# Performance work log

Measured on AMD Instinct MI355X. Metric: run time of the kernel, lower is better.

The kernel has to match this reference:

```python
import jax, jax.numpy as jnp
import numpy as np

D_MODEL = 768
N_HEADS = 12
D_K = D_MODEL // N_HEADS
EPS = 1e-5


def layer_norm(x, g, b):
    mu = jnp.mean(x, axis=-1, keepdims=True)
    var = jnp.var(x, axis=-1, keepdims=True)
    return (x - mu) * jax.lax.rsqrt(var + EPS) * g + b


def setup_inputs() -> dict:
    key = jax.random.key(0)
    ks = jax.random.split(key, 16)
    d, h = D_MODEL, 4 * D_MODEL
    s = 1.0 / np.sqrt(d)
    inp = {
        "x": jax.random.normal(ks[0], (2, 4096, d), jnp.float32),
        "wq": jax.random.normal(ks[1], (d, d), jnp.float32) * s,
        "bq": jnp.zeros((d,), jnp.float32),
        "wk": jax.random.normal(ks[2], (d, d), jnp.float32) * s,
        "bk": jnp.zeros((d,), jnp.float32),
        "wv": jax.random.normal(ks[3], (d, d), jnp.float32) * s,
        "bv": jnp.zeros((d,), jnp.float32),
        "wo": jax.random.normal(ks[4], (d, d), jnp.float32) * s,
        "bo": jnp.zeros((d,), jnp.float32),
        "w1": jax.random.normal(ks[5], (h, d), jnp.float32) * s,
        "b1": jnp.zeros((h,), jnp.float32),
        "w2": jax.random.normal(ks[6], (d, h), jnp.float32) * (1.0 / np.sqrt(h)),
        "b2": jnp.zeros((d,), jnp.float32),
        "g1": jnp.ones((d,), jnp.float32),
        "beta1": jnp.zeros((d,), jnp.float32),
        "g2": jnp.ones((d,), jnp.float32),
        "beta2": jnp.zeros((d,), jnp.float32),
    }
    return inp


def reference(x, wq, bq, wk, bk, wv, bv, wo, bo, w1, b1, w2, b2, g1, beta1, g2, beta2):
    B, S, D = x.shape
    # --- MHA (self-attention, torch Linear: y = x @ W.T + b) ---
    def heads(t):  # [B,S,D] -> [B,H,S,d_k]
        return t.reshape(B, S, N_HEADS, D_K).transpose(0, 2, 1, 3)
    q = heads(x @ wq.T + bq)
    k = heads(x @ wk.T + bk)
    v = heads(x @ wv.T + bv)
    scores = jnp.einsum("bhqd,bhkd->bhqk", q, k) / np.sqrt(D_K)
    attn = jax.nn.softmax(scores, axis=-1)
    ctx = jnp.einsum("bhqk,bhkd->bhqd", attn, v)
    ctx = ctx.transpose(0, 2, 1, 3).reshape(B, S, D)
    mha_out = ctx @ wo.T + bo
    # --- residual + LN1 ---
    n1 = layer_norm(x + mha_out, g1, beta1)
    # --- FFN (exact GELU, dropout=0/eval) ---
    hdn = jax.nn.gelu(n1 @ w1.T + b1, approximate=False)
    ffn_out = hdn @ w2.T + b2
    # --- residual + LN2 ---
    return layer_norm(n1 + ffn_out, g2, beta2)
```

## Files before the change

kernel.cpp:

```cpp
#include <hip/hip_runtime.h>
#include <cstdint>
#include <cstddef>


#define D_MODEL 768
#define N_HEADS 12
#define D_K     64
#define SEQ     4096
#define BATCH   2
#define M_ROWS  (BATCH * SEQ)
#define H_FF    3072
#define LDQKV   2304

#define QSCALE 0.18033688011112042f

typedef __bf16 bf16_t;
typedef __attribute__((ext_vector_type(8))) __bf16 bf16x8;
typedef __attribute__((ext_vector_type(4))) __bf16 bf16x4;
typedef __attribute__((ext_vector_type(2))) __bf16 bf16x2;
typedef __attribute__((ext_vector_type(4))) float  floatx4;
typedef __attribute__((ext_vector_type(4))) short  short4_t;

union bf16x4_cast { bf16x4 h; short4_t s; };

__device__ __forceinline__ float gelu_exact(float x) {
    return 0.5f * x * (1.0f + erff(x * 0.70710678118654752f));
}

#if __has_builtin(__builtin_amdgcn_exp2f)
#define EXP2F(x) __builtin_amdgcn_exp2f(x)
#else
static __device__ __forceinline__ float EXP2F(float x) {
    float r; asm("v_exp_f32 %0, %1" : "=v"(r) : "v"(x)); return r;
}
#endif

#define GLL16(gp, lp)                                                         \
    __builtin_amdgcn_global_load_lds(                                         \
        (const __attribute__((address_space(1))) void*)(gp),                  \
        (__attribute__((address_space(3))) void*)(lp), 16, 0, 0)

#define NX_V  (6291456 / 4)
#define NW_V  (589824 / 4)
#define NF_V  (2359296 / 4)
#define NCONV_V (NX_V + 4 * NW_V + 2 * NF_V)

__global__ __launch_bounds__(256) void fused_convert_kernel(
    const float* __restrict__ x,  const float* __restrict__ wq,
    const float* __restrict__ wk, const float* __restrict__ wv,
    const float* __restrict__ wo, const float* __restrict__ w1,
    const float* __restrict__ w2,
    bf16_t* __restrict__ xb, bf16_t* __restrict__ wqkvb,
    bf16_t* __restrict__ wob, bf16_t* __restrict__ w1b,
    bf16_t* __restrict__ w2b) {
    const int v = blockIdx.x * 256 + threadIdx.x;
    const float* src; bf16_t* dst; int off; float scale = 1.0f;
    if (v < NX_V)                    { src = x;  dst = xb;              off = v; }
    else if (v < NX_V + NW_V)        { src = wq; dst = wqkvb;           off = v - NX_V; scale = QSCALE; }
    else if (v < NX_V + 2 * NW_V)    { src = wk; dst = wqkvb + 589824;  off = v - NX_V - NW_V; }
    else if (v < NX_V + 3 * NW_V)    { src = wv; dst = wqkvb + 1179648; off = v - NX_V - 2 * NW_V; }
    else if (v < NX_V + 4 * NW_V)    { src = wo; dst = wob;             off = v - NX_V - 3 * NW_V; }
    else if (v < NX_V + 4 * NW_V + NF_V) { src = w1; dst = w1b;         off = v - NX_V - 4 * NW_V; }
    else                             { src = w2; dst = w2b;             off = v - NX_V - 4 * NW_V - NF_V; }
    floatx4 f = *(const floatx4*)&src[(size_t)off * 4];
    bf16x4 o = bf16x4{(bf16_t)(f[0] * scale), (bf16_t)(f[1] * scale),
                      (bf16_t)(f[2] * scale), (bf16_t)(f[3] * scale)};
    *(bf16x4*)&dst[(size_t)off * 4] = o;
}

__global__ __launch_bounds__(256) void pack_bias_kernel(
    const float* __restrict__ bq, const float* __restrict__ bk,
    const float* __restrict__ bv, float* __restrict__ dst) {
    int i = blockIdx.x * 256 + threadIdx.x;
    if (i < 768)       dst[i] = bq[i] * QSCALE;
    else if (i < 1536) dst[i] = bk[i - 768];
    else if (i < 2304) dst[i] = bv[i - 1536];
}

template<int BN>
__global__ __launch_bounds__(256) void gemm_lds_kernel(
    const bf16_t* __restrict__ A, const bf16_t* __restrict__ W,
    const float* __restrict__ bias, bf16_t* __restrict__ C,
    int M, int N, int K, int act) {

    __shared__ bf16_t As[128 * 32];
    __shared__ bf16_t Bs[BN * 32];

    const int t    = threadIdx.x;
    const int lane = t & 63;
    const int w    = t >> 6;
    const int lrow = lane & 15;
    const int quad = lane >> 4;
    const int n0   = blockIdx.x * BN;
    const int m0   = blockIdx.y * 128;

    constexpr int MI  = (BN == 128) ? 4 : 2;
    const int wmo = (BN == 128) ? (w >> 1) * 64 : w * 32;
    const int wno = (BN == 128) ? (w & 1) * 64 : 0;

    const int aidx0 = (w * 2 + 0) * 64 + lane;
    const int aidx1 = (w * 2 + 1) * 64 + lane;
    const size_t a_g0 = (size_t)(m0 + (aidx0 >> 2)) * K + (aidx0 & 3) * 8;
    const size_t a_g1 = (size_t)(m0 + (aidx1 >> 2)) * K + (aidx1 & 3) * 8;
    size_t b_g0, b_g1 = 0;
    if constexpr (BN == 128) {
        b_g0 = (size_t)(n0 + (aidx0 >> 2)) * K + (aidx0 & 3) * 8;
        b_g1 = (size_t)(n0 + (aidx1 >> 2)) * K + (aidx1 & 3) * 8;
    } else {
        const int bidx = w * 64 + lane;
        b_g0 = (size_t)(n0 + (bidx >> 2)) * K + (bidx & 3) * 8;
    }

    floatx4 acc[MI][4];
#pragma unroll
    for (int i = 0; i < MI; ++i)
#pragma unroll
        for (int j = 0; j < 4; ++j) acc[i][j] = floatx4{0.f, 0.f, 0.f, 0.f};

    for (int k0 = 0; k0 < K; k0 += 32) {
        GLL16(&A[a_g0 + k0], &As[(w * 2 + 0) * 512]);
        GLL16(&A[a_g1 + k0], &As[(w * 2 + 1) * 512]);
        if constexpr (BN == 128) {
            GLL16(&W[b_g0 + k0], &Bs[(w * 2 + 0) * 512]);
            GLL16(&W[b_g1 + k0], &Bs[(w * 2 + 1) * 512]);
        } else {
            GLL16(&W[b_g0 + k0], &Bs[w * 512]);
        }
        __syncthreads();

        bf16x8 a[MI], b[4];
#pragma unroll
        for (int i = 0; i < MI; ++i)
            a[i] = *(bf16x8*)&As[(wmo + i * 16 + lrow) * 32 + quad * 8];
#pragma unroll
        for (int j = 0; j < 4; ++j)
            b[j] = *(bf16x8*)&Bs[(wno + j * 16 + lrow) * 32 + quad * 8];
#pragma unroll
        for (int i = 0; i < MI; ++i)
#pragma unroll
            for (int j = 0; j < 4; ++j)
                acc[i][j] = __builtin_amdgcn_mfma_f32_16x16x32_bf16(a[i], b[j], acc[i][j], 0, 0, 0);
        __syncthreads();
    }

#pragma unroll
    for (int i = 0; i < MI; ++i) {
#pragma unroll
        for (int j = 0; j < 4; ++j) {
            const int n = n0 + wno + j * 16 + lrow;
            const float bv = bias[n];
#pragma unroll
            for (int r = 0; r < 4; ++r) {
                const int m = m0 + wmo + i * 16 + quad * 4 + r;
                float v = acc[i][j][r] + bv;
                if (act) v = gelu_exact(v);
                C[(size_t)m * N + n] = (bf16_t)v;
            }
        }
    }
}

__global__ __launch_bounds__(256, 3) void attn_kernel(
    const bf16_t* __restrict__ QKV, bf16_t* __restrict__ Ctx) {

    __shared__ bf16_t Ks[64 * 72];
    __shared__ bf16_t Vt[64 * 72];

    const int t    = threadIdx.x;
    const int lane = t & 63;
    const int w    = t >> 6;
    const int lrow = lane & 15;
    const int quad = lane >> 4;

    const int b  = blockIdx.y / N_HEADS;
    const int h  = blockIdx.y % N_HEADS;
    const int q0 = blockIdx.x * 128 + w * 32;
    const size_t base_q = ((size_t)b * SEQ) * LDQKV + h * D_K;
    const size_t base_k = base_q + 768;
    const size_t base_v = base_q + 1536;
    const size_t base_o = ((size_t)b * SEQ) * D_MODEL + h * D_K;

    bf16x8 qf[2][2];
#pragma unroll
    for (int s = 0; s < 2; ++s) {
        const size_t qrow = base_q + (size_t)(q0 + s * 16 + lrow) * LDQKV + quad * 8;
        qf[s][0] = *(const bf16x8*)&QKV[qrow];
        qf[s][1] = *(const bf16x8*)&QKV[qrow + 32];
    }

    float l_part[2] = {0.f, 0.f};
    floatx4 o_acc[2][4];
#pragma unroll
    for (int s = 0; s < 2; ++s)
#pragma unroll
        for (int d = 0; d < 4; ++d) o_acc[s][d] = floatx4{0.f, 0.f, 0.f, 0.f};

    const int skey = t >> 2;
    const int sch  = t & 3;
    const int kp   = t >> 3;
    const int sch8 = t & 7;
    const int vcol = ((2 * kp) & 63) ^ (sch8 << 3);

    const size_t gk0 = base_k + (size_t)skey * LDQKV + sch * 8;
    const size_t gv0 = base_v + (size_t)(2 * kp) * LDQKV + sch8 * 8;
    bf16x8 kv0 = *(const bf16x8*)&QKV[gk0];
    bf16x8 kv1 = *(const bf16x8*)&QKV[gk0 + 32];
    bf16x8 vv0 = *(const bf16x8*)&QKV[gv0];
    bf16x8 vv1 = *(const bf16x8*)&QKV[gv0 + LDQKV];

    for (int k0 = 0; k0 < SEQ; k0 += 64) {
        *(bf16x8*)&Ks[skey * 72 + sch * 8]      = kv0;
        *(bf16x8*)&Ks[skey * 72 + sch * 8 + 32] = kv1;
#pragma unroll
        for (int j = 0; j < 8; ++j)
            *(bf16x2*)&Vt[(sch8 * 8 + j) * 72 + vcol] = bf16x2{vv0[j], vv1[j]};
        __syncthreads();

        if (k0 + 64 < SEQ) {
            const size_t gk = gk0 + (size_t)(k0 + 64) * LDQKV;
            const size_t gv = gv0 + (size_t)(k0 + 64) * LDQKV;
            kv0 = *(const bf16x8*)&QKV[gk];
            kv1 = *(const bf16x8*)&QKV[gk + 32];
            vv0 = *(const bf16x8*)&QKV[gv];
            vv1 = *(const bf16x8*)&QKV[gv + LDQKV];
        }

        __builtin_amdgcn_s_setprio(1);
        short4_t p[2][4];
#pragma unroll
        for (int kt = 0; kt < 4; ++kt) {
            bf16x8 ka0 = *(bf16x8*)&Ks[(kt * 16 + lrow) * 72 + quad * 8];
            bf16x8 ka1 = *(bf16x8*)&Ks[(kt * 16 + lrow) * 72 + 32 + quad * 8];
            floatx4 z = floatx4{0.f, 0.f, 0.f, 0.f};
#pragma unroll
            for (int s = 0; s < 2; ++s) {
                floatx4 st = __builtin_amdgcn_mfma_f32_16x16x32_bf16(ka0, qf[s][0], z, 0, 0, 0);
                st = __builtin_amdgcn_mfma_f32_16x16x32_bf16(ka1, qf[s][1], st, 0, 0, 0);
                float p0 = EXP2F(st[0]), p1 = EXP2F(st[1]);
                float p2 = EXP2F(st[2]), p3 = EXP2F(st[3]);
                l_part[s] += (p0 + p1) + (p2 + p3);
                bf16x4_cast pc;
                pc.h = bf16x4{(bf16_t)p0, (bf16_t)p1, (bf16_t)p2, (bf16_t)p3};
                p[s][kt] = pc.s;
            }
        }

#pragma unroll
        for (int dt = 0; dt < 4; ++dt) {
            const int d   = dt * 16 + lrow;
            const int swv = ((d >> 3) & 7) << 3;
#pragma unroll
            for (int kc = 0; kc < 4; ++kc) {
                bf16x4_cast ac;
                ac.h = *(bf16x4*)&Vt[d * 72 + ((kc * 16 + quad * 4) ^ swv)];
                o_acc[0][dt] = __builtin_amdgcn_mfma_f32_16x16x16bf16_1k(
                    ac.s, p[0][kc], o_acc[0][dt], 0, 0, 0);
                o_acc[1][dt] = __builtin_amdgcn_mfma_f32_16x16x16bf16_1k(
                    ac.s, p[1][kc], o_acc[1][dt], 0, 0, 0);
            }
        }
        __builtin_amdgcn_s_setprio(0);
        __syncthreads();
    }

#pragma unroll
    for (int s = 0; s < 2; ++s) {
        float lsum = l_part[s];
        lsum += __shfl_xor(lsum, 16, 64);
        lsum += __shfl_xor(lsum, 32, 64);
        const float inv = 1.0f / lsum;
        const size_t orow = base_o + (size_t)(q0 + s * 16 + lrow) * D_MODEL;
#pragma unroll
        for (int dt = 0; dt < 4; ++dt) {
            bf16x4 ov = bf16x4{(bf16_t)(o_acc[s][dt][0] * inv),
                               (bf16_t)(o_acc[s][dt][1] * inv),
                               (bf16_t)(o_acc[s][dt][2] * inv),
                               (bf16_t)(o_acc[s][dt][3] * inv)};
            *(bf16x4*)&Ctx[orow + dt * 16 + quad * 4] = ov;
        }
    }
}

__global__ __launch_bounds__(256) void ln_res_f32in_kernel(
    const float* __restrict__ x, const bf16_t* __restrict__ res,
    const float* __restrict__ g, const float* __restrict__ be,
    bf16_t* __restrict__ out) {
    const int row = blockIdx.x, t = threadIdx.x;
    const size_t base = (size_t)row * D_MODEL;
    float vals[3], sum = 0.f, sq = 0.f;
#pragma unroll
    for (int it = 0; it < 3; ++it) {
        int i = t + it * 256;
        float v = x[base + i] + (float)res[base + i];
        vals[it] = v; sum += v; sq += v * v;
    }
#pragma unroll
    for (int d = 1; d < 64; d <<= 1) { sum += __shfl_xor(sum, d, 64); sq += __shfl_xor(sq, d, 64); }
    __shared__ float ssum[4], ssq[4], s_mu, s_rs;
    if ((t & 63) == 0) { ssum[t >> 6] = sum; ssq[t >> 6] = sq; }
    __syncthreads();
    if (t == 0) {
        float S = ssum[0] + ssum[1] + ssum[2] + ssum[3];
        float Qq = ssq[0] + ssq[1] + ssq[2] + ssq[3];
        float mu = S / D_MODEL;
        s_mu = mu;
        s_rs = rsqrtf(Qq / D_MODEL - mu * mu + 1e-5f);
    }
    __syncthreads();
    const float mu = s_mu, rs = s_rs;
#pragma unroll
    for (int it = 0; it < 3; ++it) {
        int i = t + it * 256;
        out[base + i] = (bf16_t)((vals[it] - mu) * rs * g[i] + be[i]);
    }
}

__global__ __launch_bounds__(256) void ln_res_final_kernel(
    const bf16_t* __restrict__ a, const bf16_t* __restrict__ bfb,
    const float* __restrict__ g, const float* __restrict__ be,
    float* __restrict__ out) {
    const int row = blockIdx.x, t = threadIdx.x;
    const size_t base = (size_t)row * D_MODEL;
    float vals[3], sum = 0.f, sq = 0.f;
#pragma unroll
    for (int it = 0; it < 3; ++it) {
        int i = t + it * 256;
        float v = (float)a[base + i] + (float)bfb[base + i];
        vals[it] = v; sum += v; sq += v * v;
    }
#pragma unroll
    for (int d = 1; d < 64; d <<= 1) { sum += __shfl_xor(sum, d, 64); sq += __shfl_xor(sq, d, 64); }
    __shared__ float ssum[4], ssq[4], s_mu, s_rs;
    if ((t & 63) == 0) { ssum[t >> 6] = sum; ssq[t >> 6] = sq; }
    __syncthreads();
    if (t == 0) {
        float S = ssum[0] + ssum[1] + ssum[2] + ssum[3];
        float Qq = ssq[0] + ssq[1] + ssq[2] + ssq[3];
        float mu = S / D_MODEL;
        s_mu = mu;
        s_rs = rsqrtf(Qq / D_MODEL - mu * mu + 1e-5f);
    }
    __syncthreads();
    const float mu = s_mu, rs = s_rs;
#pragma unroll
    for (int it = 0; it < 3; ++it) {
        int i = t + it * 256;
        out[base + i] = (vals[it] - mu) * rs * g[i] + be[i];
    }
}

extern "C" void kernel_launch(void* const* d_in, const int* in_sizes, int n_in,
                              void* d_out, int out_size, void* d_ws, size_t ws_size,
                              hipStream_t stream) {
    const float* x    = (const float*)d_in[0];
    const float* wq   = (const float*)d_in[1];
    const float* bq   = (const float*)d_in[2];
    const float* wk   = (const float*)d_in[3];
    const float* bk   = (const float*)d_in[4];
    const float* wv   = (const float*)d_in[5];
    const float* bv   = (const float*)d_in[6];
    const float* wo   = (const float*)d_in[7];
    const float* bo   = (const float*)d_in[8];
    const float* w1   = (const float*)d_in[9];
    const float* b1   = (const float*)d_in[10];
    const float* w2   = (const float*)d_in[11];
    const float* b2   = (const float*)d_in[12];
    const float* g1   = (const float*)d_in[13];
    const float* be1  = (const float*)d_in[14];
    const float* g2   = (const float*)d_in[15];
    const float* be2  = (const float*)d_in[16];
    float* out = (float*)d_out;

    char* ws = (char*)d_ws;
    const size_t SZ_XB   = (size_t)M_ROWS * D_MODEL * 2;
    const size_t SZ_QKV  = (size_t)M_ROWS * LDQKV * 2;
    const size_t SZ_CTX  = SZ_XB;
    const size_t SZ_H    = (size_t)M_ROWS * H_FF * 2;
    const size_t SZ_WQKV = (size_t)LDQKV * D_MODEL * 2;
    const size_t SZ_WO   = (size_t)D_MODEL * D_MODEL * 2;
    const size_t SZ_W1   = (size_t)H_FF * D_MODEL * 2;

    bf16_t* xb    = (bf16_t*)(ws);
    bf16_t* qkvb  = (bf16_t*)(ws + SZ_XB);
    bf16_t* ctxb  = (bf16_t*)(ws + SZ_XB + SZ_QKV);
    bf16_t* hb    = (bf16_t*)(ws + SZ_XB + SZ_QKV + SZ_CTX);
    char*   wsw   = ws + SZ_XB + SZ_QKV + SZ_CTX + SZ_H;
    bf16_t* wqkvb = (bf16_t*)(wsw);
    bf16_t* wob   = (bf16_t*)(wsw + SZ_WQKV);
    bf16_t* w1b   = (bf16_t*)(wsw + SZ_WQKV + SZ_WO);
    bf16_t* w2b   = (bf16_t*)(wsw + SZ_WQKV + SZ_WO + SZ_W1);
    float*  bqkv  = (float*)(wsw + SZ_WQKV + SZ_WO + 2 * SZ_W1);
    bf16_t* mhab  = qkvb;
    bf16_t* n1b   = xb;
    bf16_t* ffb   = ctxb;

    fused_convert_kernel<<<NCONV_V / 256, 256, 0, stream>>>(
        x, wq, wk, wv, wo, w1, w2, xb, wqkvb, wob, w1b, w2b);
    pack_bias_kernel<<<9, 256, 0, stream>>>(bq, bk, bv, bqkv);

    gemm_lds_kernel<128><<<dim3(LDQKV / 128, M_ROWS / 128), 256, 0, stream>>>(
        xb, wqkvb, bqkv, qkvb, M_ROWS, LDQKV, D_MODEL, 0);

    attn_kernel<<<dim3(SEQ / 128, BATCH * N_HEADS), 256, 0, stream>>>(qkvb, ctxb);

    gemm_lds_kernel<64><<<dim3(D_MODEL / 64, M_ROWS / 128), 256, 0, stream>>>(
        ctxb, wob, bo, mhab, M_ROWS, D_MODEL, D_MODEL, 0);

    ln_res_f32in_kernel<<<M_ROWS, 256, 0, stream>>>(x, mhab, g1, be1, n1b);

    gemm_lds_kernel<128><<<dim3(H_FF / 128, M_ROWS / 128), 256, 0, stream>>>(
        n1b, w1b, b1, hb, M_ROWS, H_FF, D_MODEL, 1);

    gemm_lds_kernel<64><<<dim3(D_MODEL / 64, M_ROWS / 128), 256, 0, stream>>>(
        hb, w2b, b2, ffb, M_ROWS, D_MODEL, H_FF, 0);

    ln_res_final_kernel<<<M_ROWS, 256, 0, stream>>>(n1b, ffb, g2, be2, out);
}
```

Baseline: 504.9 us.

## Double GEMM K-tile to 64 with XOR-swizzled LDS and vectorized epilogue

The LDS GEMM kernel now stages a 64-wide K slice per iteration instead of 32, which halves the number of barrier pairs per GEMM. Global-to-LDS loads use an XOR swizzle on the 8-element column chunks to avoid LDS bank conflicts on the 128-byte rows. The MFMA operands are swapped so each lane holds four consecutive N outputs, letting the epilogue load bias as a float4 and write bf16x4 vectors instead of scattered scalar stores. In exchange LDS use per block doubles, which may lower occupancy.

```diff
diff --git a/kernel.cpp b/kernel.cpp
--- a/kernel.cpp
+++ b/kernel.cpp
@@ -83,8 +83,8 @@
     const float* __restrict__ bias, bf16_t* __restrict__ C,
     int M, int N, int K, int act) {
 
-    __shared__ bf16_t As[128 * 32];
-    __shared__ bf16_t Bs[BN * 32];
+    __shared__ bf16_t As[128 * 64];
+    __shared__ bf16_t Bs[BN * 64];
 
     const int t    = threadIdx.x;
     const int lane = t & 63;
@@ -94,22 +94,24 @@
     const int n0   = blockIdx.x * BN;
     const int m0   = blockIdx.y * 128;
 
-    constexpr int MI  = (BN == 128) ? 4 : 2;
+    constexpr int MI = (BN == 128) ? 4 : 2;
+    constexpr int NB = (BN == 128) ? 4 : 2;
     const int wmo = (BN == 128) ? (w >> 1) * 64 : w * 32;
     const int wno = (BN == 128) ? (w & 1) * 64 : 0;
 
-    const int aidx0 = (w * 2 + 0) * 64 + lane;
-    const int aidx1 = (w * 2 + 1) * 64 + lane;
-    const size_t a_g0 = (size_t)(m0 + (aidx0 >> 2)) * K + (aidx0 & 3) * 8;
-    const size_t a_g1 = (size_t)(m0 + (aidx1 >> 2)) * K + (aidx1 & 3) * 8;
-    size_t b_g0, b_g1 = 0;
-    if constexpr (BN == 128) {
-        b_g0 = (size_t)(n0 + (aidx0 >> 2)) * K + (aidx0 & 3) * 8;
-        b_g1 = (size_t)(n0 + (aidx1 >> 2)) * K + (aidx1 & 3) * 8;
-    } else {
-        const int bidx = w * 64 + lane;
-        b_g0 = (size_t)(n0 + (bidx >> 2)) * K + (bidx & 3) * 8;
-    }
+    const int srow = lane >> 3;
+    const int scol = ((lane & 7) ^ srow) * 8;
+    size_t a_g[4];
+#pragma unroll
+    for (int i = 0; i < 4; ++i)
+        a_g[i] = (size_t)(m0 + (w * 4 + i) * 8 + srow) * K + scol;
+    size_t b_g[NB];
+#pragma unroll
+    for (int i = 0; i < NB; ++i)
+        b_g[i] = (size_t)(n0 + (w * NB + i) * 8 + srow) * K + scol;
+
+    const int slot0 = (quad ^ (lrow & 7)) * 8;
+    const int slot1 = slot0 ^ 32;
 
     floatx4 acc[MI][4];
 #pragma unroll
@@ -117,45 +119,52 @@
 #pragma unroll
         for (int j = 0; j < 4; ++j) acc[i][j] = floatx4{0.f, 0.f, 0.f, 0.f};
 
-    for (int k0 = 0; k0 < K; k0 += 32) {
-        GLL16(&A[a_g0 + k0], &As[(w * 2 + 0) * 512]);
-        GLL16(&A[a_g1 + k0], &As[(w * 2 + 1) * 512]);
-        if constexpr (BN == 128) {
-            GLL16(&W[b_g0 + k0], &Bs[(w * 2 + 0) * 512]);
-            GLL16(&W[b_g1 + k0], &Bs[(w * 2 + 1) * 512]);
-        } else {
-            GLL16(&W[b_g0 + k0], &Bs[w * 512]);
-        }
+    for (int k0 = 0; k0 < K; k0 += 64) {
+#pragma unroll
+        for (int i = 0; i < 4; ++i)
+            GLL16(&A[a_g[i] + k0], &As[(w * 4 + i) * 512]);
+#pragma unroll
+        for (int i = 0; i < NB; ++i)
+            GLL16(&W[b_g[i] + k0], &Bs[(w * NB + i) * 512]);
         __syncthreads();
 
-        bf16x8 a[MI], b[4];
-#pragma unroll
-        for (int i = 0; i < MI; ++i)
-            a[i] = *(bf16x8*)&As[(wmo + i * 16 + lrow) * 32 + quad * 8];
-#pragma unroll
-        for (int j = 0; j < 4; ++j)
-            b[j] = *(bf16x8*)&Bs[(wno + j * 16 + lrow) * 32 + quad * 8];
-#pragma unroll
-        for (int i = 0; i < MI; ++i)
+#pragma unroll
+        for (int kk = 0; kk < 2; ++kk) {
+            const int off = kk ? slot1 : slot0;
+            bf16x8 a[MI], b[4];
+#pragma unroll
+            for (int i = 0; i < MI; ++i)
+                a[i] = *(bf16x8*)&As[(wmo + i * 16 + lrow) * 64 + off];
 #pragma unroll
             for (int j = 0; j < 4; ++j)
-                acc[i][j] = __builtin_amdgcn_mfma_f32_16x16x32_bf16(a[i], b[j], acc[i][j], 0, 0, 0);
+                b[j] = *(bf16x8*)&Bs[(wno + j * 16 + lrow) * 64 + off];
+#pragma unroll
+            for (int i = 0; i < MI; ++i)
+#pragma unroll
+                for (int j = 0; j < 4; ++j)
+                    acc[i][j] = __builtin_amdgcn_mfma_f32_16x16x32_bf16(
+                        b[j], a[i], acc[i][j], 0, 0, 0);
+        }
         __syncthreads();
     }
 
 #pragma unroll
     for (int i = 0; i < MI; ++i) {
+        const int m = m0 + wmo + i * 16 + lrow;
 #pragma unroll
         for (int j = 0; j < 4; ++j) {
-            const int n = n0 + wno + j * 16 + lrow;
-            const float bv = bias[n];
-#pragma unroll
-            for (int r = 0; r < 4; ++r) {
-                const int m = m0 + wmo + i * 16 + quad * 4 + r;
-                float v = acc[i][j][r] + bv;
-                if (act) v = gelu_exact(v);
-                C[(size_t)m * N + n] = (bf16_t)v;
+            const int n = n0 + wno + j * 16 + quad * 4;
+            const floatx4 bv = *(const floatx4*)&bias[n];
+            float v0 = acc[i][j][0] + bv[0];
+            float v1 = acc[i][j][1] + bv[1];
+            float v2 = acc[i][j][2] + bv[2];
+            float v3 = acc[i][j][3] + bv[3];
+            if (act) {
+                v0 = gelu_exact(v0); v1 = gelu_exact(v1);
+                v2 = gelu_exact(v2); v3 = gelu_exact(v3);
             }
+            *(bf16x4*)&C[(size_t)m * N + n] =
+                bf16x4{(bf16_t)v0, (bf16_t)v1, (bf16_t)v2, (bf16_t)v3};
         }
     }
 }
```

Result: faster. 483.0 us (-4.3%).
